# Kernel optimization log

Hardware: AMD Instinct MI355X
Metric: run time of the kernel (lower is better)

Reference implementation:

```python
import jax, jax.numpy as jnp
import numpy as np

NUM_CAPSULES = 16
IN_DIM = 512
OUT_DIM = 32
ROUTING_ITERS = 3
EPS = 1e-08


def setup_inputs() -> dict:
    key = jax.random.key(0)
    kx, kw = jax.random.split(key)
    x = jax.random.normal(kx, (32768, IN_DIM), dtype=jnp.float32)
    W = jax.random.normal(kw, (IN_DIM, NUM_CAPSULES * OUT_DIM), dtype=jnp.float32)
    return {"x": x, "W": W}


def squash(s):
    # s: [batch, out_dim]
    norm = jnp.sum(s * s, axis=-1, keepdims=True)
    scale = norm / (1.0 + norm)
    return scale * s / (jnp.sqrt(norm) + EPS)


def reference(x, W):
    batch = x.shape[0]
    # u: [batch, num_capsules, out_dim]
    u = jnp.matmul(x, W).reshape(batch, NUM_CAPSULES, OUT_DIM)
    b = jnp.zeros((batch, NUM_CAPSULES), dtype=x.dtype)
    v = None
    for _ in range(ROUTING_ITERS):
        c = jax.nn.softmax(b, axis=1)[..., None]       # [batch, caps, 1]
        s = jnp.sum(c * u, axis=1)                      # [batch, out_dim]
        v = squash(s)                                   # [batch, out_dim]
        b = b + jnp.sum(u * v[:, None, :], axis=-1)     # [batch, caps]
    return v
```

## Files before the change

kernel.cpp:

```cpp
#include <hip/hip_runtime.h>
#include <math.h>


#define BATCH   32768
#define KDIM    512
#define NDIM    512
#define OUT_DIM 32
#define EPS_F   1e-8f
#define NKT     32
#define KPS     8
#define NSB     4

typedef _Float16 half8  __attribute__((ext_vector_type(8)));
typedef _Float16 half4t __attribute__((ext_vector_type(4)));
typedef float   floatx4 __attribute__((ext_vector_type(4)));
typedef float  floatx16 __attribute__((ext_vector_type(16)));

template <int CTRL>
__device__ __forceinline__ float dpp_mov(float x) {
    return __int_as_float(__builtin_amdgcn_mov_dpp(__float_as_int(x), CTRL, 0xF, 0xF, true));
}
template <int XMASK>
__device__ __forceinline__ float swz_xor(float x) {
    return __int_as_float(__builtin_amdgcn_ds_swizzle(__float_as_int(x), (XMASK << 10) | 31));
}
#define ROR4  0x124
#define ROR8  0x128
#define QXOR1 0xB1
#define QXOR2 0x4E

__device__ __forceinline__ float cap_sum(float x) {
    x += dpp_mov<ROR4>(x);
    x += dpp_mov<ROR8>(x);
    x += swz_xor<16>(x);
    x += __shfl_xor(x, 32);
    return x;
}
__device__ __forceinline__ float cap_max(float x) {
    x = fmaxf(x, dpp_mov<ROR4>(x));
    x = fmaxf(x, dpp_mov<ROR8>(x));
    x = fmaxf(x, swz_xor<16>(x));
    x = fmaxf(x, __shfl_xor(x, 32));
    return x;
}
__device__ __forceinline__ float dg_sum(float x) {
    x += dpp_mov<QXOR1>(x);
    x += dpp_mov<QXOR2>(x);
    return x;
}

__global__ void prep_w(const float* __restrict__ W, _Float16* __restrict__ Whl) {
    __shared__ float tile[32][33];
    const int tx = threadIdx.x, ty = threadIdx.y;
    const int n0 = blockIdx.x * 32, k0 = blockIdx.y * 32;
#pragma unroll
    for (int i = 0; i < 4; ++i)
        tile[ty + 8 * i][tx] = W[(size_t)(k0 + ty + 8 * i) * NDIM + n0 + tx];
    __syncthreads();
#pragma unroll
    for (int i = 0; i < 4; ++i) {
        const int k = k0 + tx, n = n0 + ty + 8 * i;
        const float v = tile[tx][ty + 8 * i];
        const _Float16 h = (_Float16)v;
        const _Float16 l = (_Float16)(v - (float)h);
        const size_t off = (size_t)(k >> 4) * (NDIM * 32) + (size_t)n * 32 + (k & 15);
        Whl[off]      = h;
        Whl[off + 16] = l;
    }
}

__global__ __launch_bounds__(256, 2)
void capsule_mfma(const float* __restrict__ x, const _Float16* __restrict__ Whl,
                  float* __restrict__ out) {
    __shared__ __align__(16) char smem[66560];
    float (*u_lds)[520] = (float (*)[520])smem;

    const int tid  = threadIdx.x;
    const int w    = tid >> 6;
    const int lane = tid & 63;
    const int ln = lane & 31, q = lane >> 5;
    const int rowBlk = blockIdx.x * 64;
    const int C0 = w * 128;

    floatx16 acc[2][4];
#pragma unroll
    for (int mf = 0; mf < 2; ++mf)
#pragma unroll
        for (int nt = 0; nt < 4; ++nt)
#pragma unroll
            for (int i = 0; i < 16; ++i) acc[mf][nt][i] = 0.f;

    const int srow0 = tid >> 5;
    const int sf    = tid & 31;
    const int skt   = sf >> 2;
    const int skq   = sf & 3;
    const float* aga = x + (size_t)(rowBlk + srow0) * KDIM + skt * 16 + skq * 4;
    const int ssw = (srow0 >> 1) & 3;
    const int woffh = skt * 4096 + srow0 * 64 + (((skq >> 1) ^ ssw) * 16) + (skq & 1) * 8;

    const int hoff0 = ln * 64 + ((q ^ ((ln >> 1) & 3)) * 16);

    const int lane_off = (C0 + ln) * 32 + q * 8;

    half8 bh[4], bl[4];
#pragma unroll
    for (int nt = 0; nt < 4; ++nt) {
        const _Float16* bp = Whl + nt * 1024 + lane_off;
        bh[nt] = *(const half8*)bp;
        bl[nt] = *(const half8*)(bp + 16);
    }
    {
        floatx4 s0[8];
#pragma unroll
        for (int i = 0; i < 8; ++i)
            s0[i] = __builtin_nontemporal_load((const floatx4*)(aga + (size_t)(8 * i) * KDIM));
#pragma unroll
        for (int i = 0; i < 8; ++i) {
            half4t h4, l4;
#pragma unroll
            for (int j = 0; j < 4; ++j) {
                h4[j] = (_Float16)s0[i][j];
                l4[j] = (_Float16)(s0[i][j] - (float)h4[j]);
            }
            *(half4t*)(smem + woffh + i * 512)        = h4;
            *(half4t*)(smem + (woffh ^ 32) + i * 512) = l4;
        }
    }

#define COMPUTE_KK(kk)                                                          \
    {                                                                           \
        const int kt = s * KPS + (kk);                                          \
        const char* ab = smem + abuf + (kk) * 4096;                             \
        const half8 ah0 = *(const half8*)(ab + hoff0);                          \
        const half8 al0 = *(const half8*)(ab + (hoff0 ^ 32));                   \
        const half8 ah1 = *(const half8*)(ab + hoff0 + 2048);                   \
        const half8 al1 = *(const half8*)(ab + ((hoff0 + 2048) ^ 32));          \
        const int ktn = (kt + 1 < NKT) ? kt + 1 : kt;                           \
        const _Float16* bkt = Whl + (size_t)ktn * 16384 + lane_off;             \
        _Pragma("unroll")                                                       \
        for (int nt = 0; nt < 4; ++nt) {                                        \
            acc[0][nt] = __builtin_amdgcn_mfma_f32_32x32x16_f16(ah0, bh[nt], acc[0][nt], 0, 0, 0); \
            acc[0][nt] = __builtin_amdgcn_mfma_f32_32x32x16_f16(al0, bh[nt], acc[0][nt], 0, 0, 0); \
            acc[1][nt] = __builtin_amdgcn_mfma_f32_32x32x16_f16(ah1, bh[nt], acc[1][nt], 0, 0, 0); \
            acc[1][nt] = __builtin_amdgcn_mfma_f32_32x32x16_f16(al1, bh[nt], acc[1][nt], 0, 0, 0); \
            acc[0][nt] = __builtin_amdgcn_mfma_f32_32x32x16_f16(ah0, bl[nt], acc[0][nt], 0, 0, 0); \
            acc[1][nt] = __builtin_amdgcn_mfma_f32_32x32x16_f16(ah1, bl[nt], acc[1][nt], 0, 0, 0); \
            bh[nt] = *(const half8*)(bkt + nt * 1024);                          \
            bl[nt] = *(const half8*)(bkt + nt * 1024 + 16);                     \
        }                                                                       \
    }

#define STAGE_HALF(h0)                                                          \
    {                                                                           \
        half4t h4, l4;                                                          \
        _Pragma("unroll")                                                       \
        for (int i = 0; i < 4; ++i) {                                           \
            _Pragma("unroll")                                                   \
            for (int j = 0; j < 4; ++j) {                                       \
                h4[j] = (_Float16)sv[i][j];                                     \
                l4[j] = (_Float16)(sv[i][j] - (float)h4[j]);                    \
            }                                                                   \
            *(half4t*)(smem + nbuf + woffh + ((h0) + i) * 512)        = h4;     \
            *(half4t*)(smem + nbuf + ((woffh ^ 32)) + ((h0) + i) * 512) = l4;   \
        }                                                                       \
    }

#pragma unroll 1
    for (int s = 0; s < NSB; ++s) {
        __syncthreads();
        const int abuf = (s & 1) * 32768;
        const int nbuf = abuf ^ 32768;
        floatx4 sv[4];
        if (s + 1 < NSB) {
#pragma unroll
            for (int i = 0; i < 4; ++i)
                sv[i] = __builtin_nontemporal_load(
                    (const floatx4*)(aga + (size_t)(s + 1) * 128 + (size_t)(8 * i) * KDIM));
        }
        COMPUTE_KK(0)
        COMPUTE_KK(1)
        if (s + 1 < NSB) STAGE_HALF(0)
        if (s + 1 < NSB) {
#pragma unroll
            for (int i = 0; i < 4; ++i)
                sv[i] = __builtin_nontemporal_load(
                    (const floatx4*)(aga + (size_t)(s + 1) * 128 + (size_t)(8 * (i + 4)) * KDIM));
        }
        COMPUTE_KK(2)
        COMPUTE_KK(3)
        COMPUTE_KK(4)
        COMPUTE_KK(5)
        if (s + 1 < NSB) STAGE_HALF(4)
        COMPUTE_KK(6)
        COMPUTE_KK(7)
    }

    const int dgrp = lane & 3;
#pragma unroll
    for (int p = 0; p < 2; ++p) {
        __syncthreads();
        {
            const int mf = p;
#pragma unroll
            for (int nt = 0; nt < 4; ++nt)
#pragma unroll
                for (int reg = 0; reg < 16; ++reg)
                    u_lds[(reg & 3) + 8 * (reg >> 2) + 4 * q][C0 + nt * 32 + ln] = acc[mf][nt][reg];
        }
        __syncthreads();
#pragma unroll 1
        for (int ri = 0; ri < 8; ++ri) {
            const int rl = w * 8 + ri;
            const floatx4 ua = *(const floatx4*)&u_lds[rl][lane * 8];
            const floatx4 ub = *(const floatx4*)&u_lds[rl][lane * 8 + 4];
            const float u8[8] = {ua[0], ua[1], ua[2], ua[3],
                                 ub[0], ub[1], ub[2], ub[3]};
            float b_own = 0.f;
            float v[8];
#pragma unroll
            for (int it = 0; it < 3; ++it) {
                float c_own;
                if (it == 0) {
                    c_own = 1.0f / 16.0f;
                } else {
                    const float m = cap_max(b_own);
                    const float e = __expf(b_own - m);
                    const float ssum = cap_sum(e);
                    c_own = e / ssum;
                }
                float s8[8];
#pragma unroll
                for (int j = 0; j < 8; ++j) s8[j] = c_own * u8[j];
#pragma unroll
                for (int j = 0; j < 8; ++j) s8[j] += dpp_mov<ROR4>(s8[j]);
#pragma unroll
                for (int j = 0; j < 8; ++j) s8[j] += dpp_mov<ROR8>(s8[j]);
#pragma unroll
                for (int j = 0; j < 8; ++j) s8[j] += swz_xor<16>(s8[j]);
#pragma unroll
                for (int j = 0; j < 8; ++j) s8[j] += __shfl_xor(s8[j], 32);
                float nrm = 0.f;
#pragma unroll
                for (int j = 0; j < 8; ++j) nrm = fmaf(s8[j], s8[j], nrm);
                nrm = dg_sum(nrm);
                const float scale = nrm / ((1.f + nrm) * (sqrtf(nrm) + EPS_F));
#pragma unroll
                for (int j = 0; j < 8; ++j) v[j] = scale * s8[j];
                if (it < 2) {
                    float dot = 0.f;
#pragma unroll
                    for (int j = 0; j < 8; ++j) dot = fmaf(u8[j], v[j], dot);
                    dot = dg_sum(dot);
                    b_own += dot;
                }
            }
            if (lane < 4) {
                float* o = out + (size_t)(rowBlk + p * 32 + rl) * OUT_DIM + dgrp * 8;
                floatx4 o0 = {v[0], v[1], v[2], v[3]};
                floatx4 o1 = {v[4], v[5], v[6], v[7]};
                __builtin_nontemporal_store(o0, (floatx4*)o);
                __builtin_nontemporal_store(o1, (floatx4*)(o + 4));
            }
        }
    }
}

extern "C" void kernel_launch(void* const* d_in, const int* in_sizes, int n_in,
                              void* d_out, int out_size, void* d_ws, size_t ws_size,
                              hipStream_t stream) {
    const float* x = (const float*)d_in[0];
    const float* W = (const float*)d_in[1];
    float* out = (float*)d_out;
    _Float16* Whl = (_Float16*)d_ws;

    prep_w<<<dim3(16, 16), dim3(32, 8), 0, stream>>>(W, Whl);
    capsule_mfma<<<dim3(BATCH / 64), dim3(256), 0, stream>>>(x, Whl, out);
}
```

Measured before the change: 167.0 us.

## Stage x via global_load_lds in fp32, split fp16 in-register, use 512-thread blocks

Replaces the register-staged x loads and fp16 hi/lo conversion writes to LDS with direct global-to-LDS DMA loads of raw fp32 tiles. The hi/lo split now happens after the LDS read, just before the MFMAs. The block grows to 8 waves, each owning one M-fragment, with half the accumulators and double-buffered B-fragment prefetch. The aim is to cut VGPR pressure and staging instructions and to raise occupancy, at the cost of redoing the conversion per wave and reading more LDS bytes per MFMA.

```diff
diff --git a/kernel.cpp b/kernel.cpp
--- a/kernel.cpp
+++ b/kernel.cpp
@@ -12,7 +12,6 @@
 #define NSB     4
 
 typedef _Float16 half8  __attribute__((ext_vector_type(8)));
-typedef _Float16 half4t __attribute__((ext_vector_type(4)));
 typedef float   floatx4 __attribute__((ext_vector_type(4)));
 typedef float  floatx16 __attribute__((ext_vector_type(16)));
 
@@ -48,6 +47,11 @@
     x += dpp_mov<QXOR2>(x);
     return x;
 }
+
+#define GLL16(gp, lp)                                                   \
+    __builtin_amdgcn_global_load_lds(                                   \
+        (const __attribute__((address_space(1))) void*)(gp),            \
+        (__attribute__((address_space(3))) void*)(lp), 16, 0, 0)
 
 __global__ void prep_w(const float* __restrict__ W, _Float16* __restrict__ Whl) {
     __shared__ float tile[32][33];
@@ -69,7 +73,7 @@
     }
 }
 
-__global__ __launch_bounds__(256, 2)
+__global__ __launch_bounds__(512, 4)
 void capsule_mfma(const float* __restrict__ x, const _Float16* __restrict__ Whl,
                   float* __restrict__ out) {
     __shared__ __align__(16) char smem[66560];
@@ -79,89 +83,68 @@
     const int w    = tid >> 6;
     const int lane = tid & 63;
     const int ln = lane & 31, q = lane >> 5;
+    const int mf   = w >> 2;
     const int rowBlk = blockIdx.x * 64;
-    const int C0 = w * 128;
-
-    floatx16 acc[2][4];
-#pragma unroll
-    for (int mf = 0; mf < 2; ++mf)
-#pragma unroll
-        for (int nt = 0; nt < 4; ++nt)
-#pragma unroll
-            for (int i = 0; i < 16; ++i) acc[mf][nt][i] = 0.f;
-
-    const int srow0 = tid >> 5;
-    const int sf    = tid & 31;
-    const int skt   = sf >> 2;
-    const int skq   = sf & 3;
-    const float* aga = x + (size_t)(rowBlk + srow0) * KDIM + skt * 16 + skq * 4;
-    const int ssw = (srow0 >> 1) & 3;
-    const int woffh = skt * 4096 + srow0 * 64 + (((skq >> 1) ^ ssw) * 16) + (skq & 1) * 8;
-
-    const int hoff0 = ln * 64 + ((q ^ ((ln >> 1) & 3)) * 16);
+    const int C0 = (w & 3) * 128;
+
+    floatx16 acc[4];
+#pragma unroll
+    for (int nt = 0; nt < 4; ++nt)
+#pragma unroll
+        for (int i = 0; i < 16; ++i) acc[nt][i] = 0.f;
+
+    const int srow = (tid >> 2) & 63;
+    const int sktb = tid >> 8;
+    const int scp  = tid & 3;
+    const int ssw  = (srow >> 1) & 3;
+    const float* gsrc0 = x + (size_t)(rowBlk + srow) * KDIM
+                           + sktb * 16 + (scp ^ ssw) * 4;
+
+    const int ar   = mf * 32 + ln;
+    const int asw  = (ar >> 1) & 3;
+    const int aoff0 = ar * 64 + (((2 * q)     ^ asw) * 16);
+    const int aoff1 = ar * 64 + (((2 * q + 1) ^ asw) * 16);
 
     const int lane_off = (C0 + ln) * 32 + q * 8;
 
-    half8 bh[4], bl[4];
-#pragma unroll
-    for (int nt = 0; nt < 4; ++nt) {
-        const _Float16* bp = Whl + nt * 1024 + lane_off;
-        bh[nt] = *(const half8*)bp;
-        bl[nt] = *(const half8*)(bp + 16);
-    }
+#pragma unroll
+    for (int i = 0; i < 4; ++i)
+        GLL16(gsrc0 + 32 * i, smem + tid * 16 + i * 8192);
+    half8 bh[2], bl[2];
     {
-        floatx4 s0[8];
-#pragma unroll
-        for (int i = 0; i < 8; ++i)
-            s0[i] = __builtin_nontemporal_load((const floatx4*)(aga + (size_t)(8 * i) * KDIM));
-#pragma unroll
-        for (int i = 0; i < 8; ++i) {
-            half4t h4, l4;
-#pragma unroll
-            for (int j = 0; j < 4; ++j) {
-                h4[j] = (_Float16)s0[i][j];
-                l4[j] = (_Float16)(s0[i][j] - (float)h4[j]);
-            }
-            *(half4t*)(smem + woffh + i * 512)        = h4;
-            *(half4t*)(smem + (woffh ^ 32) + i * 512) = l4;
-        }
+        const _Float16* bp = Whl + lane_off;
+        bh[0] = *(const half8*)bp;
+        bl[0] = *(const half8*)(bp + 16);
     }
 
 #define COMPUTE_KK(kk)                                                          \
     {                                                                           \
         const int kt = s * KPS + (kk);                                          \
         const char* ab = smem + abuf + (kk) * 4096;                             \
-        const half8 ah0 = *(const half8*)(ab + hoff0);                          \
-        const half8 al0 = *(const half8*)(ab + (hoff0 ^ 32));                   \
-        const half8 ah1 = *(const half8*)(ab + hoff0 + 2048);                   \
-        const half8 al1 = *(const half8*)(ab + ((hoff0 + 2048) ^ 32));          \
+        const floatx4 af0 = *(const floatx4*)(ab + aoff0);                      \
+        const floatx4 af1 = *(const floatx4*)(ab + aoff1);                      \
+        half8 ah, al;                                                           \
+        _Pragma("unroll")                                                       \
+        for (int j = 0; j < 4; ++j) {                                           \
+            const float f0 = af0[j], f1 = af1[j];                               \
+            const _Float16 h0 = (_Float16)f0, h1 = (_Float16)f1;                \
+            ah[j] = h0;  ah[j + 4] = h1;                                        \
+            al[j]     = (_Float16)(f0 - (float)h0);                            \
+            al[j + 4] = (_Float16)(f1 - (float)h1);                            \
+        }                                                                       \
         const int ktn = (kt + 1 < NKT) ? kt + 1 : kt;                           \
-        const _Float16* bkt = Whl + (size_t)ktn * 16384 + lane_off;             \
+        const _Float16* bkt_cur = Whl + (size_t)kt  * 16384 + lane_off;         \
+        const _Float16* bkt_nxt = Whl + (size_t)ktn * 16384 + lane_off;         \
         _Pragma("unroll")                                                       \
         for (int nt = 0; nt < 4; ++nt) {                                        \
-            acc[0][nt] = __builtin_amdgcn_mfma_f32_32x32x16_f16(ah0, bh[nt], acc[0][nt], 0, 0, 0); \
-            acc[0][nt] = __builtin_amdgcn_mfma_f32_32x32x16_f16(al0, bh[nt], acc[0][nt], 0, 0, 0); \
-            acc[1][nt] = __builtin_amdgcn_mfma_f32_32x32x16_f16(ah1, bh[nt], acc[1][nt], 0, 0, 0); \
-            acc[1][nt] = __builtin_amdgcn_mfma_f32_32x32x16_f16(al1, bh[nt], acc[1][nt], 0, 0, 0); \
-            acc[0][nt] = __builtin_amdgcn_mfma_f32_32x32x16_f16(ah0, bl[nt], acc[0][nt], 0, 0, 0); \
-            acc[1][nt] = __builtin_amdgcn_mfma_f32_32x32x16_f16(ah1, bl[nt], acc[1][nt], 0, 0, 0); \
-            bh[nt] = *(const half8*)(bkt + nt * 1024);                          \
-            bl[nt] = *(const half8*)(bkt + nt * 1024 + 16);                     \
-        }                                                                       \
-    }
-
-#define STAGE_HALF(h0)                                                          \
-    {                                                                           \
-        half4t h4, l4;                                                          \
-        _Pragma("unroll")                                                       \
-        for (int i = 0; i < 4; ++i) {                                           \
-            _Pragma("unroll")                                                   \
-            for (int j = 0; j < 4; ++j) {                                       \
-                h4[j] = (_Float16)sv[i][j];                                     \
-                l4[j] = (_Float16)(sv[i][j] - (float)h4[j]);                    \
-            }                                                                   \
-            *(half4t*)(smem + nbuf + woffh + ((h0) + i) * 512)        = h4;     \
-            *(half4t*)(smem + nbuf + ((woffh ^ 32)) + ((h0) + i) * 512) = l4;   \
+            const int cu = nt & 1, nx = cu ^ 1;                                 \
+            const _Float16* bn = (nt < 3) ? (bkt_cur + (nt + 1) * 1024)         \
+                                          : bkt_nxt;                            \
+            bh[nx] = *(const half8*)bn;                                         \
+            bl[nx] = *(const half8*)(bn + 16);                                  \
+            acc[nt] = __builtin_amdgcn_mfma_f32_32x32x16_f16(ah, bh[cu], acc[nt], 0, 0, 0); \
+            acc[nt] = __builtin_amdgcn_mfma_f32_32x32x16_f16(al, bh[cu], acc[nt], 0, 0, 0); \
+            acc[nt] = __builtin_amdgcn_mfma_f32_32x32x16_f16(ah, bl[cu], acc[nt], 0, 0, 0); \
         }                                                                       \
     }
 
@@ -170,27 +153,18 @@
         __syncthreads();
         const int abuf = (s & 1) * 32768;
         const int nbuf = abuf ^ 32768;
-        floatx4 sv[4];
         if (s + 1 < NSB) {
+            const float* g = gsrc0 + (s + 1) * 128;
 #pragma unroll
             for (int i = 0; i < 4; ++i)
-                sv[i] = __builtin_nontemporal_load(
-                    (const floatx4*)(aga + (size_t)(s + 1) * 128 + (size_t)(8 * i) * KDIM));
+                GLL16(g + 32 * i, smem + nbuf + tid * 16 + i * 8192);
         }
         COMPUTE_KK(0)
         COMPUTE_KK(1)
-        if (s + 1 < NSB) STAGE_HALF(0)
-        if (s + 1 < NSB) {
-#pragma unroll
-            for (int i = 0; i < 4; ++i)
-                sv[i] = __builtin_nontemporal_load(
-                    (const floatx4*)(aga + (size_t)(s + 1) * 128 + (size_t)(8 * (i + 4)) * KDIM));
-        }
         COMPUTE_KK(2)
         COMPUTE_KK(3)
         COMPUTE_KK(4)
         COMPUTE_KK(5)
-        if (s + 1 < NSB) STAGE_HALF(4)
         COMPUTE_KK(6)
         COMPUTE_KK(7)
     }
@@ -199,18 +173,17 @@
 #pragma unroll
     for (int p = 0; p < 2; ++p) {
         __syncthreads();
-        {
-            const int mf = p;
+        if (mf == p) {
 #pragma unroll
             for (int nt = 0; nt < 4; ++nt)
 #pragma unroll
                 for (int reg = 0; reg < 16; ++reg)
-                    u_lds[(reg & 3) + 8 * (reg >> 2) + 4 * q][C0 + nt * 32 + ln] = acc[mf][nt][reg];
+                    u_lds[(reg & 3) + 8 * (reg >> 2) + 4 * q][C0 + nt * 32 + ln] = acc[nt][reg];
         }
         __syncthreads();
 #pragma unroll 1
-        for (int ri = 0; ri < 8; ++ri) {
-            const int rl = w * 8 + ri;
+        for (int ri = 0; ri < 4; ++ri) {
+            const int rl = w * 4 + ri;
             const floatx4 ua = *(const floatx4*)&u_lds[rl][lane * 8];
             const floatx4 ub = *(const floatx4*)&u_lds[rl][lane * 8 + 4];
             const float u8[8] = {ua[0], ua[1], ua[2], ua[3],
@@ -274,5 +247,5 @@
     _Float16* Whl = (_Float16*)d_ws;
 
     prep_w<<<dim3(16, 16), dim3(32, 8), 0, stream>>>(W, Whl);
-    capsule_mfma<<<dim3(BATCH / 64), dim3(256), 0, stream>>>(x, Whl, out);
-}
+    capsule_mfma<<<dim3(BATCH / 64), dim3(512), 0, stream>>>(x, Whl, out);
+}
```

Result: no change. 167.4 us (+0.2%).

## Use 128-row blocks with 8 waves, ping-pong W registers and barrier-phased MFMA

Applied to the files above, without the earlier changes.

Each block now covers 128 rows with 512 threads (8 waves). Waves split into two 64-row halves, so every W fragment pulled into registers serves twice as many rows and global W traffic per row drops. The K loop now runs as barrier-separated phases with double-buffered B registers, s_setprio around the MFMA bursts, and x staging spread across the phases. This adds barriers and register pressure, and the occupancy target rises to two 512-thread blocks per CU. The routing epilogue now runs four passes of four rows per wave.

```diff
diff --git a/kernel.cpp b/kernel.cpp
--- a/kernel.cpp
+++ b/kernel.cpp
@@ -8,8 +8,9 @@
 #define OUT_DIM 32
 #define EPS_F   1e-8f
 #define NKT     32
-#define KPS     8
-#define NSB     4
+#define KPS     4
+#define NSB     8
+#define ROWS    128
 
 typedef _Float16 half8  __attribute__((ext_vector_type(8)));
 typedef _Float16 half4t __attribute__((ext_vector_type(4)));
@@ -69,7 +70,7 @@
     }
 }
 
-__global__ __launch_bounds__(256, 2)
+__global__ __launch_bounds__(512, 2)
 void capsule_mfma(const float* __restrict__ x, const _Float16* __restrict__ Whl,
                   float* __restrict__ out) {
     __shared__ __align__(16) char smem[66560];
@@ -79,8 +80,9 @@
     const int w    = tid >> 6;
     const int lane = tid & 63;
     const int ln = lane & 31, q = lane >> 5;
-    const int rowBlk = blockIdx.x * 64;
-    const int C0 = w * 128;
+    const int rowBlk = blockIdx.x * ROWS;
+    const int rb = (w >> 2) * 64;
+    const int C0 = (w & 3) * 128;
 
     floatx16 acc[2][4];
 #pragma unroll
@@ -90,78 +92,95 @@
 #pragma unroll
             for (int i = 0; i < 16; ++i) acc[mf][nt][i] = 0.f;
 
-    const int srow0 = tid >> 5;
-    const int sf    = tid & 31;
-    const int skt   = sf >> 2;
-    const int skq   = sf & 3;
-    const float* aga = x + (size_t)(rowBlk + srow0) * KDIM + skt * 16 + skq * 4;
-    const int ssw = (srow0 >> 1) & 3;
-    const int woffh = skt * 4096 + srow0 * 64 + (((skq >> 1) ^ ssw) * 16) + (skq & 1) * 8;
-
-    const int hoff0 = ln * 64 + ((q ^ ((ln >> 1) & 3)) * 16);
+    const int srow = tid >> 2;
+    const int skq  = tid & 3;
+    const int ssw  = (srow >> 1) & 3;
+    const float* aga = x + (size_t)(rowBlk + srow) * KDIM + skq * 4;
+    const int woffs = srow * 64 + (((skq >> 1) ^ ssw) * 16) + (skq & 1) * 8;
+
+    const int r0 = rb + ln;
+    const int hoff0 = r0 * 64 + ((q ^ ((r0 >> 1) & 3)) * 16);
 
     const int lane_off = (C0 + ln) * 32 + q * 8;
 
-    half8 bh[4], bl[4];
+    half8 bh0[4], bl0[4], bh1[4], bl1[4];
 #pragma unroll
     for (int nt = 0; nt < 4; ++nt) {
         const _Float16* bp = Whl + nt * 1024 + lane_off;
-        bh[nt] = *(const half8*)bp;
-        bl[nt] = *(const half8*)(bp + 16);
+        bh0[nt] = *(const half8*)bp;
+        bl0[nt] = *(const half8*)(bp + 16);
     }
     {
-        floatx4 s0[8];
-#pragma unroll
-        for (int i = 0; i < 8; ++i)
-            s0[i] = __builtin_nontemporal_load((const floatx4*)(aga + (size_t)(8 * i) * KDIM));
-#pragma unroll
-        for (int i = 0; i < 8; ++i) {
+        floatx4 s0[4];
+#pragma unroll
+        for (int i = 0; i < 4; ++i)
+            s0[i] = *(const floatx4*)(aga + (size_t)i * 16);
+#pragma unroll
+        for (int i = 0; i < 4; ++i) {
             half4t h4, l4;
 #pragma unroll
             for (int j = 0; j < 4; ++j) {
                 h4[j] = (_Float16)s0[i][j];
                 l4[j] = (_Float16)(s0[i][j] - (float)h4[j]);
             }
-            *(half4t*)(smem + woffh + i * 512)        = h4;
-            *(half4t*)(smem + (woffh ^ 32) + i * 512) = l4;
+            *(half4t*)(smem + woffs + i * 8192)        = h4;
+            *(half4t*)(smem + (woffs ^ 32) + i * 8192) = l4;
         }
     }
 
-#define COMPUTE_KK(kk)                                                          \
+#define MFMA24(AH0, AL0, AH1, AL1, BH, BL)                                      \
+    _Pragma("unroll")                                                           \
+    for (int nt = 0; nt < 4; ++nt) {                                            \
+        acc[0][nt] = __builtin_amdgcn_mfma_f32_32x32x16_f16(AH0, BH[nt], acc[0][nt], 0, 0, 0); \
+        acc[0][nt] = __builtin_amdgcn_mfma_f32_32x32x16_f16(AL0, BH[nt], acc[0][nt], 0, 0, 0); \
+        acc[1][nt] = __builtin_amdgcn_mfma_f32_32x32x16_f16(AH1, BH[nt], acc[1][nt], 0, 0, 0); \
+        acc[1][nt] = __builtin_amdgcn_mfma_f32_32x32x16_f16(AL1, BH[nt], acc[1][nt], 0, 0, 0); \
+        acc[0][nt] = __builtin_amdgcn_mfma_f32_32x32x16_f16(AH0, BL[nt], acc[0][nt], 0, 0, 0); \
+        acc[1][nt] = __builtin_amdgcn_mfma_f32_32x32x16_f16(AH1, BL[nt], acc[1][nt], 0, 0, 0); \
+    }
+
+#define PHASE(kk, BHC, BLC, BHN, BLN, STG)                                      \
     {                                                                           \
         const int kt = s * KPS + (kk);                                          \
-        const char* ab = smem + abuf + (kk) * 4096;                             \
+        const int ktn = (kt + 1 < NKT) ? kt + 1 : kt;                           \
+        const _Float16* bkt = Whl + (size_t)ktn * 16384 + lane_off;             \
+        _Pragma("unroll")                                                       \
+        for (int nt = 0; nt < 4; ++nt) {                                        \
+            BHN[nt] = *(const half8*)(bkt + nt * 1024);                         \
+            BLN[nt] = *(const half8*)(bkt + nt * 1024 + 16);                    \
+        }                                                                       \
+        const char* ab = smem + abuf + (kk) * 8192;                             \
         const half8 ah0 = *(const half8*)(ab + hoff0);                          \
         const half8 al0 = *(const half8*)(ab + (hoff0 ^ 32));                   \
         const half8 ah1 = *(const half8*)(ab + hoff0 + 2048);                   \
         const half8 al1 = *(const half8*)(ab + ((hoff0 + 2048) ^ 32));          \
-        const int ktn = (kt + 1 < NKT) ? kt + 1 : kt;                           \
-        const _Float16* bkt = Whl + (size_t)ktn * 16384 + lane_off;             \
+        STG;                                                                    \
+        __builtin_amdgcn_s_barrier();                                           \
+        __builtin_amdgcn_s_setprio(1);                                          \
+        MFMA24(ah0, al0, ah1, al1, BHC, BLC)                                    \
+        __builtin_amdgcn_s_setprio(0);                                          \
+        __builtin_amdgcn_s_barrier();                                           \
+    }
+
+#define STG_NONE ((void)0)
+#define STG_LOAD                                                                \
+    if (s + 1 < NSB) {                                                          \
         _Pragma("unroll")                                                       \
-        for (int nt = 0; nt < 4; ++nt) {                                        \
-            acc[0][nt] = __builtin_amdgcn_mfma_f32_32x32x16_f16(ah0, bh[nt], acc[0][nt], 0, 0, 0); \
-            acc[0][nt] = __builtin_amdgcn_mfma_f32_32x32x16_f16(al0, bh[nt], acc[0][nt], 0, 0, 0); \
-            acc[1][nt] = __builtin_amdgcn_mfma_f32_32x32x16_f16(ah1, bh[nt], acc[1][nt], 0, 0, 0); \
-            acc[1][nt] = __builtin_amdgcn_mfma_f32_32x32x16_f16(al1, bh[nt], acc[1][nt], 0, 0, 0); \
-            acc[0][nt] = __builtin_amdgcn_mfma_f32_32x32x16_f16(ah0, bl[nt], acc[0][nt], 0, 0, 0); \
-            acc[1][nt] = __builtin_amdgcn_mfma_f32_32x32x16_f16(ah1, bl[nt], acc[1][nt], 0, 0, 0); \
-            bh[nt] = *(const half8*)(bkt + nt * 1024);                          \
-            bl[nt] = *(const half8*)(bkt + nt * 1024 + 16);                     \
-        }                                                                       \
-    }
-
-#define STAGE_HALF(h0)                                                          \
-    {                                                                           \
-        half4t h4, l4;                                                          \
+        for (int i = 0; i < 4; ++i)                                             \
+            sv[i] = *(const floatx4*)(aga + (size_t)((s + 1) * 4 + i) * 16);    \
+    }
+#define STG_CW(i0)                                                              \
+    if (s + 1 < NSB) {                                                          \
         _Pragma("unroll")                                                       \
-        for (int i = 0; i < 4; ++i) {                                           \
+        for (int i = (i0); i < (i0) + 2; ++i) {                                 \
+            half4t h4, l4;                                                      \
             _Pragma("unroll")                                                   \
             for (int j = 0; j < 4; ++j) {                                       \
                 h4[j] = (_Float16)sv[i][j];                                     \
                 l4[j] = (_Float16)(sv[i][j] - (float)h4[j]);                    \
             }                                                                   \
-            *(half4t*)(smem + nbuf + woffh + ((h0) + i) * 512)        = h4;     \
-            *(half4t*)(smem + nbuf + ((woffh ^ 32)) + ((h0) + i) * 512) = l4;   \
+            *(half4t*)(smem + nbuf + woffs + i * 8192)        = h4;             \
+            *(half4t*)(smem + nbuf + (woffs ^ 32) + i * 8192) = l4;             \
         }                                                                       \
     }
 
@@ -171,46 +190,27 @@
         const int abuf = (s & 1) * 32768;
         const int nbuf = abuf ^ 32768;
         floatx4 sv[4];
-        if (s + 1 < NSB) {
-#pragma unroll
-            for (int i = 0; i < 4; ++i)
-                sv[i] = __builtin_nontemporal_load(
-                    (const floatx4*)(aga + (size_t)(s + 1) * 128 + (size_t)(8 * i) * KDIM));
-        }
-        COMPUTE_KK(0)
-        COMPUTE_KK(1)
-        if (s + 1 < NSB) STAGE_HALF(0)
-        if (s + 1 < NSB) {
-#pragma unroll
-            for (int i = 0; i < 4; ++i)
-                sv[i] = __builtin_nontemporal_load(
-                    (const floatx4*)(aga + (size_t)(s + 1) * 128 + (size_t)(8 * (i + 4)) * KDIM));
-        }
-        COMPUTE_KK(2)
-        COMPUTE_KK(3)
-        COMPUTE_KK(4)
-        COMPUTE_KK(5)
-        if (s + 1 < NSB) STAGE_HALF(4)
-        COMPUTE_KK(6)
-        COMPUTE_KK(7)
+        PHASE(0, bh0, bl0, bh1, bl1, STG_LOAD)
+        PHASE(1, bh1, bl1, bh0, bl0, STG_NONE)
+        PHASE(2, bh0, bl0, bh1, bl1, STG_CW(0))
+        PHASE(3, bh1, bl1, bh0, bl0, STG_CW(2))
     }
 
     const int dgrp = lane & 3;
 #pragma unroll
-    for (int p = 0; p < 2; ++p) {
+    for (int p = 0; p < 4; ++p) {
         __syncthreads();
-        {
-            const int mf = p;
+        if ((w >> 2) == (p >> 1)) {
 #pragma unroll
             for (int nt = 0; nt < 4; ++nt)
 #pragma unroll
                 for (int reg = 0; reg < 16; ++reg)
-                    u_lds[(reg & 3) + 8 * (reg >> 2) + 4 * q][C0 + nt * 32 + ln] = acc[mf][nt][reg];
+                    u_lds[(reg & 3) + 8 * (reg >> 2) + 4 * q][C0 + nt * 32 + ln] = acc[p & 1][nt][reg];
         }
         __syncthreads();
 #pragma unroll 1
-        for (int ri = 0; ri < 8; ++ri) {
-            const int rl = w * 8 + ri;
+        for (int ri = 0; ri < 4; ++ri) {
+            const int rl = w * 4 + ri;
             const floatx4 ua = *(const floatx4*)&u_lds[rl][lane * 8];
             const floatx4 ub = *(const floatx4*)&u_lds[rl][lane * 8 + 4];
             const float u8[8] = {ua[0], ua[1], ua[2], ua[3],
@@ -274,5 +274,5 @@
     _Float16* Whl = (_Float16*)d_ws;
 
     prep_w<<<dim3(16, 16), dim3(32, 8), 0, stream>>>(W, Whl);
-    capsule_mfma<<<dim3(BATCH / 64), dim3(256), 0, stream>>>(x, Whl, out);
-}
+    capsule_mfma<<<dim3(BATCH / ROWS), dim3(512), 0, stream>>>(x, Whl, out);
+}
```

Result: faster. 158.5 us (-5.1%).
